# Kernel tuning notes

Measured on AMD Instinct MI355X. Metric: run time of the kernel, lower is better.

The kernel has to match this reference:

```python
import jax, jax.numpy as jnp
import numpy as np

N_CHANNELS = 512
GROUPS = 8
EPS = 1e-5


def setup_inputs() -> dict:
    key = jax.random.key(0)
    ks = jax.random.split(key, 7)
    B, C, L = 8, N_CHANNELS, 4096
    s = 1.0 / np.sqrt(C)
    return {
        "x": jax.random.normal(ks[0], (B, C, L), dtype=jnp.float32),
        "gamma": jnp.ones((C,), dtype=jnp.float32),
        "beta": jnp.zeros((C,), dtype=jnp.float32),
        "w_qkv": jax.random.normal(ks[1], (3 * C, C), dtype=jnp.float32) * s,
        "b_qkv": jax.random.normal(ks[2], (3 * C,), dtype=jnp.float32) * 0.01,
        "w_out": jax.random.normal(ks[3], (C, C), dtype=jnp.float32) * s,
        "b_out": jax.random.normal(ks[4], (C,), dtype=jnp.float32) * 0.01,
    }


def group_norm(x, gamma, beta):
    # x: [B, C, L]; normalize per group of C//GROUPS channels over (channels_in_group, L)
    B, C, L = x.shape
    xg = x.reshape(B, GROUPS, C // GROUPS, L)
    mean = xg.mean(axis=(2, 3), keepdims=True)
    var = xg.var(axis=(2, 3), keepdims=True)
    xn = ((xg - mean) * jax.lax.rsqrt(var + EPS)).reshape(B, C, L)
    return xn * gamma[None, :, None] + beta[None, :, None]


def reference(x, gamma, beta, w_qkv, b_qkv, w_out, b_out):
    B, C, L = x.shape
    xn = group_norm(x, gamma, beta)
    # 1x1 conv == channel matmul: [3C, C] @ [B, C, L] -> [B, 3C, L]
    qkv = jnp.einsum('oc,bcl->bol', w_qkv, xn) + b_qkv[None, :, None]
    q, k, v = jnp.split(qkv, 3, axis=1)  # each [B, C, L]
    scale = C ** (-0.5)
    attn = jnp.einsum('bcl,bck->blk', q, k) * scale  # [B, L, L]
    attn = jax.nn.softmax(attn, axis=-1)
    out = jnp.einsum('blk,bck->bcl', attn, v)  # [B, C, L]
    proj = jnp.einsum('oc,bcl->bol', w_out, out) + b_out[None, :, None]
    return x + proj
```

## Files before the change

### kernel.cpp

```cpp
#include <hip/hip_runtime.h>

typedef __attribute__((ext_vector_type(4))) float f32x4;
typedef __attribute__((ext_vector_type(8))) short short8;
typedef unsigned short u16;
typedef unsigned int u32;

static constexpr int Bb = 8, Cc = 512, Ll = 4096;

__device__ __forceinline__ u16 f2bf(float f) {
  u32 u = __builtin_bit_cast(u32, f);
  u = (u + 0x7FFFu + ((u >> 16) & 1u)) >> 16;
  return (u16)u;
}

__device__ __forceinline__ void load_lds16(const void* g, void* l) {
  __builtin_amdgcn_global_load_lds((const __attribute__((address_space(1))) void*)g,
                                   (__attribute__((address_space(3))) void*)l,
                                   16, 0, 0);
}

__global__ void cvt_bf16_kernel(const float* __restrict__ src, u16* __restrict__ dst, int n) {
  int stride = gridDim.x * blockDim.x;
  for (int i = blockIdx.x * blockDim.x + threadIdx.x; i < n; i += stride)
    dst[i] = f2bf(src[i]);
}

__global__ __launch_bounds__(256)
void gn_stats_kernel(const float* __restrict__ x, float* __restrict__ stats) {
  int bg = blockIdx.x;
  const f32x4* p = (const f32x4*)(x + (size_t)bg * (64 * Ll));
  float s = 0.f, ss = 0.f;
  for (int i = threadIdx.x; i < 64 * Ll / 4; i += 256) {
    f32x4 v = p[i];
    s  += v[0] + v[1] + v[2] + v[3];
    ss += v[0]*v[0] + v[1]*v[1] + v[2]*v[2] + v[3]*v[3];
  }
  __shared__ float rs[256], rq[256];
  rs[threadIdx.x] = s; rq[threadIdx.x] = ss;
  __syncthreads();
  for (int st = 128; st > 0; st >>= 1) {
    if (threadIdx.x < st) { rs[threadIdx.x] += rs[threadIdx.x + st]; rq[threadIdx.x] += rq[threadIdx.x + st]; }
    __syncthreads();
  }
  if (threadIdx.x == 0) {
    const float inv_n = 1.f / (64.f * 4096.f);
    float mean = rs[0] * inv_n;
    float var  = rq[0] * inv_n - mean * mean;
    stats[bg * 2]     = mean;
    stats[bg * 2 + 1] = rsqrtf(var + 1e-5f);
  }
}

__global__ __launch_bounds__(256)
void gn_apply_t_kernel(const float* __restrict__ x, const float* __restrict__ gamma,
                       const float* __restrict__ beta, const float* __restrict__ stats,
                       u16* __restrict__ xn_t) {
  int lt = blockIdx.x;
  int ct = blockIdx.y;
  int b  = blockIdx.z;
  __shared__ float tile[64][65];
  int t = threadIdx.x;
  int lx = t & 63;
  int qd = t >> 6;
  int c0 = ct * 64, l0 = lt * 64;
  float mean = stats[(b * 8 + ct) * 2];
  float rstd = stats[(b * 8 + ct) * 2 + 1];
  #pragma unroll
  for (int i = 0; i < 16; ++i) {
    int cl = qd + i * 4;
    int c = c0 + cl;
    float v = x[((size_t)b * Cc + c) * Ll + l0 + lx];
    tile[cl][lx] = (v - mean) * rstd * gamma[c] + beta[c];
  }
  __syncthreads();
  #pragma unroll
  for (int i = 0; i < 16; ++i) {
    int ll = qd + i * 4;
    xn_t[((size_t)b * Ll + l0 + ll) * Cc + c0 + lx] = f2bf(tile[lx][ll]);
  }
}

template <int MODE>
__global__ __launch_bounds__(256, 2)
void gemm_tn(const u16* __restrict__ A, long long aStride, int lda,
             const u16* __restrict__ Bm, long long bStride, int ldb,
             void* __restrict__ Dv, long long dStride, int ldd,
             const float* __restrict__ bias, const float* __restrict__ resid, int K) {
  int z = blockIdx.z;
  A  += (size_t)z * aStride;
  Bm += (size_t)z * bStride;
  int m0 = blockIdx.x * 128, n0 = blockIdx.y * 128;
  __shared__ uint4 sA[1024], sB[1024];
  int tid = threadIdx.x, lane = tid & 63;
  int wv = tid >> 6, wr = wv >> 1, wc = wv & 1;
  int l15 = lane & 15, l4 = lane >> 4;
  f32x4 acc[4][4] = {};
  for (int kt = 0; kt < K; kt += 64) {
    __syncthreads();
    #pragma unroll
    for (int p = 0; p < 4; ++p) {
      int s = p * 256 + tid;
      int r = ((s >> 7) << 4) | (((s >> 2) & 1) << 3) | ((s >> 3) & 7);
      int g = (((s >> 6) & 1) << 2) | (s & 3);
      load_lds16(A  + (size_t)(m0 + r) * lda + kt + g * 8, &sA[s]);
      load_lds16(Bm + (size_t)(n0 + r) * ldb + kt + g * 8, &sB[s]);
    }
    __syncthreads();
    #pragma unroll
    for (int ks = 0; ks < 2; ++ks) {
      short8 af[4], bfr[4];
      #pragma unroll
      for (int i = 0; i < 4; ++i) {
        int sa = (4 * wr + i) * 128 + ks * 64 + (l15 & 7) * 8 + (l15 >> 3) * 4 + l4;
        af[i]  = *(const short8*)&sA[sa];
        int sb = (4 * wc + i) * 128 + ks * 64 + (l15 & 7) * 8 + (l15 >> 3) * 4 + l4;
        bfr[i] = *(const short8*)&sB[sb];
      }
      #pragma unroll
      for (int i = 0; i < 4; ++i)
        #pragma unroll
        for (int j = 0; j < 4; ++j)
          acc[i][j] = __builtin_amdgcn_mfma_f32_16x16x32_bf16(af[i], bfr[j], acc[i][j], 0, 0, 0);
    }
  }
  #pragma unroll
  for (int i = 0; i < 4; ++i) {
    #pragma unroll
    for (int j = 0; j < 4; ++j) {
      #pragma unroll
      for (int r = 0; r < 4; ++r) {
        int m = m0 + 64 * wr + 16 * i + 4 * l4 + r;
        int n = n0 + 64 * wc + 16 * j + l15;
        float val = acc[i][j][r] + (MODE == 0 ? bias[n] : bias[m]);
        size_t idx = (size_t)z * dStride + (size_t)m * ldd + n;
        if (MODE == 2) ((float*)Dv)[idx] = val + resid[idx];
        else           ((u16*)Dv)[idx]   = f2bf(val);
      }
    }
  }
}

__global__ __launch_bounds__(512, 2)
void flash_attn_kernel(const u16* __restrict__ qk_t, const u16* __restrict__ v,
                       u16* __restrict__ o_t) {
  int bid = blockIdx.x;
  int b  = bid & 7;
  int q0 = (bid >> 3) * 128;
  int tid = threadIdx.x, lane = tid & 63, wv = tid >> 6;
  int l15 = lane & 15, l4 = lane >> 4;
  const u16* qkb = qk_t + (size_t)b * Ll * 1024;
  const u16* vb  = v    + (size_t)b * Cc * Ll;
  u16* ob        = o_t  + (size_t)b * Ll * Cc;

  __shared__ uint4 sK[2][32 * 64];
  __shared__ uint4 sV[2][512 * 4];
  __shared__ __align__(16) char sP[128 * 80];
  __shared__ __align__(16) float sAl[128];

  int ow_q = wv >> 2, ow_c = wv & 3;

  short8 aq[16];
  {
    const u16* qp = qkb + (size_t)(q0 + wv * 16 + l15) * 1024 + 8 * l4;
    #pragma unroll
    for (int ks = 0; ks < 16; ++ks) aq[ks] = *(const short8*)(qp + 32 * ks);
  }

  auto issueK = [&](int kt, int buf) {
    #pragma unroll
    for (int p = 0; p < 4; ++p) {
      int s = p * 512 + tid;
      int kr = (((s >> 6) & 1) << 4) | (((s >> 2) & 1) << 3) | ((s >> 3) & 7);
      int g  = ((s >> 7) << 2) | (s & 3);
      load_lds16(qkb + (size_t)(kt * 32 + kr) * 1024 + 512 + g * 8, &sK[buf][s]);
    }
  };
  auto issueV = [&](int kt, int buf) {
    #pragma unroll
    for (int p = 0; p < 4; ++p) {
      int s = p * 512 + tid;
      int r = s >> 2, g = s & 3, gw = g ^ ((r >> 1) & 3);
      load_lds16(vb + (size_t)r * Ll + kt * 32 + gw * 8, &sV[buf][s]);
    }
  };
  issueK(0, 0);
  issueV(0, 0);

  f32x4 accO[4][8];
  #pragma unroll
  for (int i = 0; i < 4; ++i)
    #pragma unroll
    for (int j = 0; j < 8; ++j) accO[i][j] = (f32x4){0.f, 0.f, 0.f, 0.f};
  float mrun = -1e30f, lrun = 0.f;
  const float scale = 0.044194173824159216f;

  const int NT = Ll / 32;
  for (int kt = 0; kt < NT; ++kt) {
    int buf = kt & 1;
    __syncthreads();
    if (kt + 1 < NT) { issueK(kt + 1, buf ^ 1); issueV(kt + 1, buf ^ 1); }

    const uint4* kb = &sK[buf][0];
    f32x4 s2[2];
    #pragma unroll
    for (int t = 0; t < 2; ++t) {
      s2[t] = (f32x4){0.f, 0.f, 0.f, 0.f};
      #pragma unroll
      for (int ks = 0; ks < 16; ++ks) {
        short8 ak = *(const short8*)&kb[ks * 128 + t * 64 + (l15 & 7) * 8 + (l15 >> 3) * 4 + l4];
        s2[t] = __builtin_amdgcn_mfma_f32_16x16x32_bf16(ak, aq[ks], s2[t], 0, 0, 0);
      }
    }

    #pragma unroll
    for (int t = 0; t < 2; ++t)
      #pragma unroll
      for (int r = 0; r < 4; ++r) s2[t][r] *= scale;
    float mx = fmaxf(fmaxf(s2[0][0], s2[0][1]), fmaxf(s2[0][2], s2[0][3]));
    mx = fmaxf(mx, fmaxf(fmaxf(s2[1][0], s2[1][1]), fmaxf(s2[1][2], s2[1][3])));
    mx = fmaxf(mx, __shfl_xor(mx, 16));
    mx = fmaxf(mx, __shfl_xor(mx, 32));
    float mnew = fmaxf(mrun, mx);
    float al = __expf(mrun - mnew);
    mrun = mnew;
    float ps = 0.f;
    #pragma unroll
    for (int t = 0; t < 2; ++t)
      #pragma unroll
      for (int r = 0; r < 4; ++r) { float pv = __expf(s2[t][r] - mnew); s2[t][r] = pv; ps += pv; }
    ps += __shfl_xor(ps, 16);
    ps += __shfl_xor(ps, 32);
    lrun = lrun * al + ps;

    {
      char* pb = sP + (16 * wv + l15) * 80;
      #pragma unroll
      for (int t = 0; t < 2; ++t) {
        u32 lo = (u32)f2bf(s2[t][0]) | ((u32)f2bf(s2[t][1]) << 16);
        u32 hi = (u32)f2bf(s2[t][2]) | ((u32)f2bf(s2[t][3]) << 16);
        uint2 w = {lo, hi};
        *(uint2*)(pb + 32 * t + 8 * l4) = w;
      }
      if (lane < 16) sAl[16 * wv + lane] = al;
    }

    __builtin_amdgcn_sched_barrier(0);
    asm volatile("s_waitcnt lgkmcnt(0)" ::: "memory");
    __builtin_amdgcn_s_barrier();
    __builtin_amdgcn_sched_barrier(0);

    #pragma unroll
    for (int i = 0; i < 4; ++i) {
      f32x4 av = *(const f32x4*)&sAl[64 * ow_q + 16 * i + 4 * l4];
      #pragma unroll
      for (int j = 0; j < 8; ++j) {
        #pragma unroll
        for (int r = 0; r < 4; ++r) accO[i][j][r] *= av[r];
      }
    }
    short8 ap[4];
    #pragma unroll
    for (int i = 0; i < 4; ++i) {
      int ra = 64 * ow_q + 16 * i + l15;
      ap[i] = *(const short8*)(sP + ra * 80 + 16 * l4);
    }
    const uint4* vbuf = &sV[buf][0];
    #pragma unroll
    for (int j = 0; j < 8; ++j) {
      int crow = 128 * ow_c + 16 * j + l15;
      short8 bv = *(const short8*)&vbuf[crow * 4 + (l4 ^ ((crow >> 1) & 3))];
      #pragma unroll
      for (int i = 0; i < 4; ++i)
        accO[i][j] = __builtin_amdgcn_mfma_f32_16x16x32_bf16(ap[i], bv, accO[i][j], 0, 0, 0);
    }
  }

  __syncthreads();
  if (lane < 16) sAl[16 * wv + lane] = lrun;
  __syncthreads();
  #pragma unroll
  for (int i = 0; i < 4; ++i) {
    f32x4 lv = *(const f32x4*)&sAl[64 * ow_q + 16 * i + 4 * l4];
    #pragma unroll
    for (int r = 0; r < 4; ++r) lv[r] = 1.f / lv[r];
    #pragma unroll
    for (int j = 0; j < 8; ++j) {
      #pragma unroll
      for (int r = 0; r < 4; ++r) {
        int q = q0 + 64 * ow_q + 16 * i + 4 * l4 + r;
        int c = 128 * ow_c + 16 * j + l15;
        ob[(size_t)q * Cc + c] = f2bf(accO[i][j][r] * lv[r]);
      }
    }
  }
}

extern "C" void kernel_launch(void* const* d_in, const int* in_sizes, int n_in,
                              void* d_out, int out_size, void* d_ws, size_t ws_size,
                              hipStream_t stream) {
  const float* x     = (const float*)d_in[0];
  const float* gamma = (const float*)d_in[1];
  const float* beta  = (const float*)d_in[2];
  const float* w_qkv = (const float*)d_in[3];
  const float* b_qkv = (const float*)d_in[4];
  const float* w_out = (const float*)d_in[5];
  const float* b_out = (const float*)d_in[6];
  float* out = (float*)d_out;

  char* ws = (char*)d_ws;
  size_t off = 0;
  auto alloc = [&](size_t bytes) -> char* {
    char* p = ws + off;
    off += (bytes + 1023) & ~(size_t)1023;
    return p;
  };
  float* stats = (float*)alloc(64 * 2 * sizeof(float));
  u16* wqb = (u16*)alloc((size_t)1536 * 512 * 2);
  u16* wob = (u16*)alloc((size_t)512 * 512 * 2);
  u16* xnt = (u16*)alloc((size_t)Bb * Ll * Cc * 2);
  u16* qkt = (u16*)alloc((size_t)Bb * Ll * 1024 * 2);
  u16* vbf = (u16*)alloc((size_t)Bb * Cc * Ll * 2);
  u16* ot  = xnt;
  if (off > ws_size) return;

  cvt_bf16_kernel<<<256, 256, 0, stream>>>(w_qkv, wqb, 1536 * 512);
  cvt_bf16_kernel<<<256, 256, 0, stream>>>(w_out, wob, 512 * 512);
  gn_stats_kernel<<<64, 256, 0, stream>>>(x, stats);
  gn_apply_t_kernel<<<dim3(64, 8, 8), 256, 0, stream>>>(x, gamma, beta, stats, xnt);
  gemm_tn<0><<<dim3(32, 8, 8), 256, 0, stream>>>(
      xnt, (long long)Ll * Cc, Cc, wqb, 0, Cc,
      qkt, (long long)Ll * 1024, 1024, b_qkv, nullptr, Cc);
  gemm_tn<1><<<dim3(4, 32, 8), 256, 0, stream>>>(
      wqb + (size_t)1024 * 512, 0, Cc, xnt, (long long)Ll * Cc, Cc,
      vbf, (long long)Cc * Ll, Ll, b_qkv + 1024, nullptr, Cc);
  flash_attn_kernel<<<256, 512, 0, stream>>>(qkt, vbf, ot);
  gemm_tn<2><<<dim3(4, 32, 8), 256, 0, stream>>>(
      wob, 0, Cc, ot, (long long)Ll * Cc, Cc,
      out, (long long)Cc * Ll, Ll, b_out, x, Cc);
}
```

Measured before the change: 668.2 us.

## Quantize Q and K to FP8 E4M3 and use FP8 MFMA for attention scores

```diff
diff --git a/kernel.cpp b/kernel.cpp
--- a/kernel.cpp
+++ b/kernel.cpp
@@ -4,6 +4,7 @@
 typedef __attribute__((ext_vector_type(8))) short short8;
 typedef unsigned short u16;
 typedef unsigned int u32;
+typedef unsigned char u8;
 
 static constexpr int Bb = 8, Cc = 512, Ll = 4096;
 
@@ -11,6 +12,22 @@
   u32 u = __builtin_bit_cast(u32, f);
   u = (u + 0x7FFFu + ((u >> 16) & 1u)) >> 16;
   return (u16)u;
+}
+
+__device__ __forceinline__ u8 f2e4m3(float f) {
+  u32 u = __builtin_bit_cast(u32, f);
+  u8 s = (u >> 24) & 0x80;
+  float af = __builtin_fabsf(f);
+  if (af >= 448.f) return s | 0x7E;
+  if (af < 0.015625f) {
+    int n = (int)rintf(af * 512.f);
+    return s | (u8)n;
+  }
+  u32 b = u & 0x7FFFFFFF;
+  u32 r = b + 0x7FFFF + ((b >> 20) & 1);
+  int e = (int)(r >> 23) - 127;
+  if (e > 8) return s | 0x7E;
+  return s | (u8)(((e + 7) << 3) | ((r >> 20) & 7));
 }
 
 __device__ __forceinline__ void load_lds16(const void* g, void* l) {
@@ -131,48 +148,53 @@
       for (int r = 0; r < 4; ++r) {
         int m = m0 + 64 * wr + 16 * i + 4 * l4 + r;
         int n = n0 + 64 * wc + 16 * j + l15;
-        float val = acc[i][j][r] + (MODE == 0 ? bias[n] : bias[m]);
-        size_t idx = (size_t)z * dStride + (size_t)m * ldd + n;
-        if (MODE == 2) ((float*)Dv)[idx] = val + resid[idx];
-        else           ((u16*)Dv)[idx]   = f2bf(val);
+        float val = acc[i][j][r] + ((MODE == 0 || MODE == 3) ? bias[n] : bias[m]);
+        if (MODE == 3) {
+          u8* base = (n < 512) ? (u8*)Dv : (u8*)const_cast<float*>(resid);
+          base[(size_t)z * dStride + (size_t)m * ldd + (n & 511)] = f2e4m3(val);
+        } else {
+          size_t idx = (size_t)z * dStride + (size_t)m * ldd + n;
+          if (MODE == 2)      ((float*)Dv)[idx] = val + resid[idx];
+          else                ((u16*)Dv)[idx]   = f2bf(val);
+        }
       }
     }
   }
 }
 
 __global__ __launch_bounds__(512, 2)
-void flash_attn_kernel(const u16* __restrict__ qk_t, const u16* __restrict__ v,
-                       u16* __restrict__ o_t) {
+void flash_attn_kernel(const u8* __restrict__ q8, const u8* __restrict__ k8,
+                       const u16* __restrict__ v, u16* __restrict__ o_t) {
   int bid = blockIdx.x;
   int b  = bid & 7;
   int q0 = (bid >> 3) * 128;
   int tid = threadIdx.x, lane = tid & 63, wv = tid >> 6;
   int l15 = lane & 15, l4 = lane >> 4;
-  const u16* qkb = qk_t + (size_t)b * Ll * 1024;
-  const u16* vb  = v    + (size_t)b * Cc * Ll;
-  u16* ob        = o_t  + (size_t)b * Ll * Cc;
-
-  __shared__ uint4 sK[2][32 * 64];
+  const u8* q8b = q8 + (size_t)b * Ll * 512;
+  const u8* k8b = k8 + (size_t)b * Ll * 512;
+  const u16* vb = v   + (size_t)b * Cc * Ll;
+  u16* ob       = o_t + (size_t)b * Ll * Cc;
+
+  __shared__ uint4 sK[2][1024];
   __shared__ uint4 sV[2][512 * 4];
   __shared__ __align__(16) char sP[128 * 80];
   __shared__ __align__(16) float sAl[128];
 
   int ow_q = wv >> 2, ow_c = wv & 3;
 
-  short8 aq[16];
+  long aq[16];
   {
-    const u16* qp = qkb + (size_t)(q0 + wv * 16 + l15) * 1024 + 8 * l4;
-    #pragma unroll
-    for (int ks = 0; ks < 16; ++ks) aq[ks] = *(const short8*)(qp + 32 * ks);
+    const u8* qp = q8b + (size_t)(q0 + wv * 16 + l15) * 512 + 8 * l4;
+    #pragma unroll
+    for (int ks = 0; ks < 16; ++ks) aq[ks] = *(const long*)(qp + 32 * ks);
   }
 
   auto issueK = [&](int kt, int buf) {
     #pragma unroll
-    for (int p = 0; p < 4; ++p) {
+    for (int p = 0; p < 2; ++p) {
       int s = p * 512 + tid;
-      int kr = (((s >> 6) & 1) << 4) | (((s >> 2) & 1) << 3) | ((s >> 3) & 7);
-      int g  = ((s >> 7) << 2) | (s & 3);
-      load_lds16(qkb + (size_t)(kt * 32 + kr) * 1024 + 512 + g * 8, &sK[buf][s]);
+      int r = s >> 5, g = s & 31;
+      load_lds16(k8b + (size_t)(kt * 32 + r) * 512 + ((g ^ (r & 15)) << 4), &sK[buf][s]);
     }
   };
   auto issueV = [&](int kt, int buf) {
@@ -200,15 +222,17 @@
     __syncthreads();
     if (kt + 1 < NT) { issueK(kt + 1, buf ^ 1); issueV(kt + 1, buf ^ 1); }
 
-    const uint4* kb = &sK[buf][0];
+    const u8* kb = (const u8*)&sK[buf][0];
     f32x4 s2[2];
     #pragma unroll
     for (int t = 0; t < 2; ++t) {
       s2[t] = (f32x4){0.f, 0.f, 0.f, 0.f};
+      int row = 16 * t + l15;
       #pragma unroll
       for (int ks = 0; ks < 16; ++ks) {
-        short8 ak = *(const short8*)&kb[ks * 128 + t * 64 + (l15 & 7) * 8 + (l15 >> 3) * 4 + l4];
-        s2[t] = __builtin_amdgcn_mfma_f32_16x16x32_bf16(ak, aq[ks], s2[t], 0, 0, 0);
+        int gr = (2 * ks + (l4 >> 1)) ^ (row & 15);
+        long ak = *(const long*)(kb + row * 512 + (gr << 4) + 8 * (l4 & 1));
+        s2[t] = __builtin_amdgcn_mfma_f32_16x16x32_fp8_fp8(ak, aq[ks], s2[t], 0, 0, 0);
       }
     }
 
@@ -318,7 +342,8 @@
   u16* wqb = (u16*)alloc((size_t)1536 * 512 * 2);
   u16* wob = (u16*)alloc((size_t)512 * 512 * 2);
   u16* xnt = (u16*)alloc((size_t)Bb * Ll * Cc * 2);
-  u16* qkt = (u16*)alloc((size_t)Bb * Ll * 1024 * 2);
+  u8*  q8  = (u8*)alloc((size_t)Bb * Ll * 512);
+  u8*  k8  = (u8*)alloc((size_t)Bb * Ll * 512);
   u16* vbf = (u16*)alloc((size_t)Bb * Cc * Ll * 2);
   u16* ot  = xnt;
   if (off > ws_size) return;
@@ -327,13 +352,13 @@
   cvt_bf16_kernel<<<256, 256, 0, stream>>>(w_out, wob, 512 * 512);
   gn_stats_kernel<<<64, 256, 0, stream>>>(x, stats);
   gn_apply_t_kernel<<<dim3(64, 8, 8), 256, 0, stream>>>(x, gamma, beta, stats, xnt);
-  gemm_tn<0><<<dim3(32, 8, 8), 256, 0, stream>>>(
+  gemm_tn<3><<<dim3(32, 8, 8), 256, 0, stream>>>(
       xnt, (long long)Ll * Cc, Cc, wqb, 0, Cc,
-      qkt, (long long)Ll * 1024, 1024, b_qkv, nullptr, Cc);
+      q8, (long long)Ll * 512, 512, b_qkv, (const float*)k8, Cc);
   gemm_tn<1><<<dim3(4, 32, 8), 256, 0, stream>>>(
       wqb + (size_t)1024 * 512, 0, Cc, xnt, (long long)Ll * Cc, Cc,
       vbf, (long long)Cc * Ll, Ll, b_qkv + 1024, nullptr, Cc);
-  flash_attn_kernel<<<256, 512, 0, stream>>>(qkt, vbf, ot);
+  flash_attn_kernel<<<256, 512, 0, stream>>>(q8, k8, vbf, ot);
   gemm_tn<2><<<dim3(4, 32, 8), 256, 0, stream>>>(
       wob, 0, Cc, ot, (long long)Ll * Cc, Cc,
       out, (long long)Cc * Ll, Ll, b_out, x, Cc);
```

New measurement: 642.5 us (median of 2 runs). -3.8%, faster.
